# Kernel optimization log

Measured on AMD Instinct MI355X. Metric: run time of the kernel, lower is better.

Reference implementation:

```python
import jax
import jax.numpy as jnp
import numpy as np
from jax import lax

DIM = 512
B, T = 8, 2048
DT = 1.0
DT_REF = 1.0
MAX_GROWTH = 0.3


def _xavier(key, shape):
    fan_in, fan_out = shape[1], shape[0]
    lim = float(np.sqrt(6.0 / (fan_in + fan_out)))
    return jax.random.uniform(key, shape, jnp.float32, -lim, lim)


def setup_inputs() -> dict:
    key = jax.random.key(0)
    ks = jax.random.split(key, 10)
    D = DIM
    return {
        "x": jax.random.normal(ks[0], (B, T, D), jnp.float32),
        # ComplexSVDTransform params (U basis is unused by the transform matrix)
        "v_raw_re": jax.random.normal(ks[1], (D, D), jnp.float32) * 0.02,
        "v_raw_im": jax.random.normal(ks[2], (D, D), jnp.float32) * 0.02,
        "log_sigma": jnp.zeros((D,), jnp.float32),
        "dft_weight": jnp.zeros((), jnp.float32),
        # GlobalFluxTracker params (gate_net only used in forward_step; not here)
        "decay_re": jax.random.normal(ks[3], (D,), jnp.float32) * 0.1 - 1.0,
        "decay_im": jax.random.normal(ks[4], (D,), jnp.float32) * 0.1,
        "mix_w": _xavier(ks[5], (2 * D, 2 * D)),
        "mix_b": jnp.zeros((2 * D,), jnp.float32),
        "proj_w": _xavier(ks[6], (2 * D, 2 * D)),
        "proj_b": jnp.zeros((2 * D,), jnp.float32),
        # TemporalPropagator eigenvalue params
        "lam_re": jax.random.normal(ks[7], (D,), jnp.float32) * 0.01,
        "lam_im": jax.random.normal(ks[8], (D,), jnp.float32) * 0.1,
    }


def _cayley(raw_re, raw_im):
    # Q = (I + A_skew)^{-1} (I - A_skew), A_skew = A - A^H
    A = raw_re + 1j * raw_im
    A_skew = A - A.conj().T
    I = jnp.eye(A.shape[0], dtype=A.dtype)
    return jnp.linalg.solve(I + A_skew, I - A_skew)


def _transform_matrix(v_raw_re, v_raw_im, log_sigma, dft_weight):
    V = _cayley(v_raw_re, v_raw_im)
    S = jnp.exp(log_sigma)
    d = v_raw_re.shape[0]
    n = jnp.arange(d, dtype=jnp.float32)
    k = n[:, None]
    dft = jnp.exp(-2j * jnp.pi * (n * k) / d) / jnp.sqrt(jnp.asarray(d, jnp.float32))
    alpha = jax.nn.sigmoid(dft_weight).astype(jnp.complex64)
    V_scaled = V * S[None, :].astype(V.dtype)  # V @ diag(S)
    return V_scaled * (1.0 - alpha) + dft.astype(jnp.complex64) * alpha


def _scan_combine(c1, c2):
    # s_t = a_t * s_{t-1} + b_t  -> associative combine (later element is c2)
    a1, b1 = c1
    a2, b2 = c2
    return (a1 * a2, b1 * a2 + b2)


def reference(x, v_raw_re, v_raw_im, log_sigma, dft_weight,
              decay_re, decay_im, mix_w, mix_b, proj_w, proj_b,
              lam_re, lam_im):
    D = x.shape[-1]
    # --- encode ---
    W = _transform_matrix(v_raw_re, v_raw_im, log_sigma, dft_weight)  # [D,D] complex
    h = jnp.einsum('btd,de->bte', x.astype(jnp.complex64), W)  # [B,T,D] complex
    # --- flux tracker operators ---
    decay = jax.nn.sigmoid(decay_re) + 1j * decay_im  # [D]
    x_cat = jnp.concatenate([h.real, h.imag], axis=-1)  # [B,T,2D]
    x_in = x_cat @ mix_w.T + mix_b
    x_re, x_im = x_in[..., :D], x_in[..., D:]
    X = x_re + 1j * x_im  # forcing [B,T,D]
    A = jnp.broadcast_to(decay.astype(jnp.complex64), h.shape)  # [B,T,D]
    # --- complex diagonal SSM recurrence via parallel scan ---
    _, states = lax.associative_scan(_scan_combine, (A, X.astype(jnp.complex64)), axis=1)
    # --- project states to source ---
    s_cat = jnp.concatenate([states.real, states.imag], axis=-1)
    s_out = s_cat @ proj_w.T + proj_b
    source = s_out[..., :D] + 1j * s_out[..., D:]
    # --- closed-form transition operators ---
    lam = jnp.clip(lam_re, -MAX_GROWTH, MAX_GROWTH) + 1j * lam_im  # [D]
    exp_arg = lam * (DT / DT_REF)
    t_decay = jnp.exp(exp_arg)
    lam_safe = lam + 1e-8 * jnp.sign(lam.real + 1e-12)
    forcing = (jnp.exp(exp_arg) - 1.0) / lam_safe
    h_out = h * t_decay + source * forcing  # [B,T,D]
    # --- decode ---
    W_inv = jnp.linalg.inv(W)
    x_out = jnp.einsum('btd,de->bte', h_out, W_inv)
    return x_out.real


if __name__ == "__main__":
    out = reference(**setup_inputs())
    print(out.shape, out.dtype)
```

## Files before the change

### kernel.cpp

```cpp
#include <hip/hip_runtime.h>
#include <hip/hip_bf16.h>

typedef unsigned short u16;
typedef _Float16 f16x8 __attribute__((ext_vector_type(8)));
typedef float f32x4 __attribute__((ext_vector_type(4)));

#define DEV __device__ __forceinline__

DEV u16 f2h(float f) { _Float16 h = (_Float16)f; u16 u; __builtin_memcpy(&u, &h, 2); return u; }
DEV float h2f(u16 u) { _Float16 h; __builtin_memcpy(&h, &u, 2); return (float)h; }
DEV void splitf(float v, u16& hi, u16& lo) { hi = f2h(v); lo = f2h(v - h2f(hi)); }
DEV float sigm(float x) { return 1.f / (1.f + __expf(-x)); }
DEV void gload16(const u16* g, u16* l) {
  __builtin_amdgcn_global_load_lds((const __attribute__((address_space(1))) void*)g,
                                   (__attribute__((address_space(3))) void*)l, 16, 0, 0);
}

static const int TT = 2048;

static const size_t OFF_AUG    = 0;
static const size_t OFF_WMAT   = OFF_AUG    + (size_t)512*1024*16;
static const size_t OFF_BINV   = OFF_WMAT   + (size_t)512*512*16;
static const size_t OFF_PIV    = OFF_BINV   + (size_t)64*64*16;
static const size_t OFF_TAB    = OFF_PIV    + (size_t)64*1024*16;
static const size_t OFF_WCATH  = OFF_TAB    + (size_t)512*32;
static const size_t OFF_WCATL  = OFF_WCATH  + (size_t)512*1024*2;
static const size_t OFF_MIXH   = OFF_WCATL  + (size_t)512*1024*2;
static const size_t OFF_MIXL   = OFF_MIXH   + (size_t)1024*1024*2;
static const size_t OFF_PROJH  = OFF_MIXL   + (size_t)1024*1024*2;
static const size_t OFF_PROJL  = OFF_PROJH  + (size_t)1024*1024*2;
static const size_t OFF_B1TH   = OFF_PROJL  + (size_t)1024*1024*2;
static const size_t OFF_B1TL   = OFF_B1TH   + (size_t)512*1024*2;
static const size_t OFF_B2TH   = OFF_B1TL   + (size_t)512*1024*2;
static const size_t OFF_B2TL   = OFF_B2TH   + (size_t)512*1024*2;
static const size_t OFF_BTMIXH = OFF_B2TL   + (size_t)512*1024*2;
static const size_t OFF_BTMIXL = OFF_BTMIXH + (size_t)1024*512*2;
static const size_t OFF_BTFH   = OFF_BTMIXL + (size_t)1024*512*2;
static const size_t OFF_BTFL   = OFF_BTFH   + (size_t)512*1536*2;
static const size_t OFF_BIAS2  = OFF_BTFL   + (size_t)512*1536*2;
static const size_t OFF_CARRY  = OFF_BIAS2  + (size_t)512*4;
static const size_t OFF_PREF   = OFF_CARRY  + (size_t)4096*16*8;
static const size_t OFF_XINF   = OFF_PREF   + (size_t)4096*16*8;
static const size_t OFF_ACATH  = OFF_XINF   + (size_t)16384*1024*4;
static const size_t OFF_ACATL  = OFF_ACATH  + (size_t)16384*1536*2;

__global__ __launch_bounds__(256) void k_split_f32(const float* __restrict__ s, u16* __restrict__ dh,
                                                   u16* __restrict__ dl, int n4) {
  int g = blockIdx.x * 256 + threadIdx.x;
  if (g >= n4) return;
  float4 v = ((const float4*)s)[g];
  ushort4 h, l;
  splitf(v.x, h.x, l.x); splitf(v.y, h.y, l.y); splitf(v.z, h.z, l.z); splitf(v.w, h.w, l.w);
  ((ushort4*)dh)[g] = h;
  ((ushort4*)dl)[g] = l;
}

__global__ __launch_bounds__(256) void k_x_to_acat(const float* __restrict__ x, u16* __restrict__ ah,
                                                   u16* __restrict__ al) {
  int g = blockIdx.x * 256 + threadIdx.x;
  if (g >= 2097152) return;
  float4 v = ((const float4*)x)[g];
  int idx = g * 4;
  int row = idx >> 9, col = idx & 511;
  ushort4 h, l;
  splitf(v.x, h.x, l.x); splitf(v.y, h.y, l.y); splitf(v.z, h.z, l.z); splitf(v.w, h.w, l.w);
  *(ushort4*)(ah + (size_t)row*1536 + col) = h;
  *(ushort4*)(al + (size_t)row*1536 + col) = l;
}

__global__ __launch_bounds__(256) void k_transpose_1024(const float* __restrict__ in, u16* __restrict__ oh,
                                                        u16* __restrict__ ol) {
  __shared__ float s[64][65];
  int lx = threadIdx.x & 63, ly = threadIdx.x >> 6;
#pragma unroll
  for (int i = 0; i < 16; ++i) {
    int c = blockIdx.y*64 + ly*16 + i;
    s[ly*16 + i][lx] = in[(size_t)c*1024 + blockIdx.x*64 + lx];
  }
  __syncthreads();
#pragma unroll
  for (int i = 0; i < 16; ++i) {
    int j = blockIdx.x*64 + ly*16 + i;
    u16 h, l; splitf(s[lx][ly*16 + i], h, l);
    oh[(size_t)j*1024 + blockIdx.y*64 + lx] = h;
    ol[(size_t)j*1024 + blockIdx.y*64 + lx] = l;
  }
}

__global__ __launch_bounds__(256) void k_build_aug_f(const float* __restrict__ vre, const float* __restrict__ vim,
                                                     float2* __restrict__ aug) {
  int g = blockIdx.x * 256 + threadIdx.x;
  if (g >= 512*1024) return;
  int i = g >> 10, j = g & 1023;
  int jc = j & 511;
  float sre = vre[i*512 + jc] - vre[jc*512 + i];
  float sim = vim[i*512 + jc] + vim[jc*512 + i];
  float idd = (i == jc) ? 1.f : 0.f;
  aug[g] = (j < 512) ? make_float2(idd + sre, sim) : make_float2(idd - sre, -sim);
}

template<typename T2, typename TR>
__global__ __launch_bounds__(1024) void gj_inv64_p(const T2* __restrict__ AUG, T2* __restrict__ BINV, int k0) {
  __shared__ T2 mcol[2][64];
  __shared__ T2 praw[2][68];
  const int tid = threadIdx.x;
  const int r = tid >> 4, q = tid & 15;
  T2 a[4];
  const T2* src = AUG + (size_t)(k0 + r)*1024 + k0 + q*4;
#pragma unroll
  for (int jj = 0; jj < 4; ++jj) a[jj] = src[jj];
  if (q == 0) mcol[0][r] = a[0];
  if (r == 0) {
#pragma unroll
    for (int jj = 0; jj < 4; ++jj) { int j = q*4 + jj; praw[0][j + (j >> 4)] = a[jj]; }
  }
  __syncthreads();
  for (int p = 0; p < 64; ++p) {
    const int bu = p & 1;
    T2 pd = praw[bu][p + (p >> 4)];
    TR inv = TR(1) / (pd.x*pd.x + pd.y*pd.y);
    T2 pinv; pinv.x = pd.x*inv; pinv.y = -pd.y*inv;
    T2 mraw = mcol[bu][r];
    T2 g; g.x = mraw.x*pinv.x - mraw.y*pinv.y; g.y = mraw.x*pinv.y + mraw.y*pinv.x;
    if (r == p) {
#pragma unroll
      for (int jj = 0; jj < 4; ++jj) {
        int j = q*4 + jj;
        T2 v;
        if (j == p) v = pinv;
        else { T2 pr = praw[bu][j + (j >> 4)]; v.x = pr.x*pinv.x - pr.y*pinv.y; v.y = pr.x*pinv.y + pr.y*pinv.x; }
        a[jj] = v;
      }
    } else {
#pragma unroll
      for (int jj = 0; jj < 4; ++jj) {
        int j = q*4 + jj;
        if (j == p) { a[jj].x = -g.x; a[jj].y = -g.y; }
        else {
          T2 pr = praw[bu][j + (j >> 4)];
          a[jj].x -= g.x*pr.x - g.y*pr.y;
          a[jj].y -= g.x*pr.y + g.y*pr.x;
        }
      }
    }
    if (p < 63) {
      const int nbu = bu ^ 1;
      if (q == ((p + 1) >> 2)) {
        const int loc = (p + 1) & 3;
#pragma unroll
        for (int jj = 0; jj < 4; ++jj) if (jj == loc) mcol[nbu][r] = a[jj];
      }
      if (r == p + 1) {
#pragma unroll
        for (int jj = 0; jj < 4; ++jj) { int j = q*4 + jj; praw[nbu][j + (j >> 4)] = a[jj]; }
      }
    }
    __syncthreads();
  }
  T2* dst = BINV + (size_t)r*64 + q*4;
#pragma unroll
  for (int jj = 0; jj < 4; ++jj) dst[jj] = a[jj];
}

template<typename T2>
__global__ __launch_bounds__(256) void gj_trans_t(const T2* __restrict__ AUG, const T2* __restrict__ BINV,
                                                  T2* __restrict__ PIV, int k0) {
  __shared__ T2 binv[64][16];
  int tid = threadIdx.x;
  int col  = k0 + 64 + blockIdx.x*64 + (tid & 63);
  int rsub = tid >> 6;
  T2 acc[16];
#pragma unroll
  for (int i = 0; i < 16; ++i) { acc[i].x = 0; acc[i].y = 0; }
  for (int kc = 0; kc < 4; ++kc) {
    for (int l = tid; l < 1024; l += 256) {
      int rr = l >> 4, cc = l & 15;
      binv[rr][cc] = BINV[(size_t)rr*64 + kc*16 + cc];
    }
    __syncthreads();
#pragma unroll 4
    for (int kk = 0; kk < 16; ++kk) {
      T2 av = AUG[(size_t)(k0 + kc*16 + kk)*1024 + col];
#pragma unroll
      for (int i = 0; i < 16; ++i) {
        T2 bv = binv[rsub*16 + i][kk];
        acc[i].x += bv.x*av.x - bv.y*av.y;
        acc[i].y += bv.x*av.y + bv.y*av.x;
      }
    }
    __syncthreads();
  }
#pragma unroll
  for (int i = 0; i < 16; ++i) PIV[(size_t)(rsub*16 + i)*1024 + col] = acc[i];
}

template<typename T2>
__global__ __launch_bounds__(256) void gj_update_t(T2* __restrict__ AUG, const T2* __restrict__ PIV, int k0) {
  __shared__ T2 mult[16][64];
  __shared__ T2 pivc[16][64];
  int tid = threadIdx.x;
  int rb = blockIdx.y;
  int colBase = k0 + 64 + blockIdx.x*64;
  for (int l = tid; l < 1024; l += 256) {
    int rr = l >> 6, kk = l & 63;
    mult[rr][kk] = AUG[(size_t)(rb*16 + rr)*1024 + k0 + kk];
  }
  int ccl = tid & 63, rsub = tid >> 6;
  int col = colBase + ccl;
  T2 acc[4];
#pragma unroll
  for (int i = 0; i < 4; ++i) acc[i] = AUG[(size_t)(rb*16 + rsub*4 + i)*1024 + col];
  for (int kc = 0; kc < 4; ++kc) {
    for (int l = tid; l < 1024; l += 256) {
      int rr = l >> 6, cc = l & 63;
      pivc[rr][cc] = PIV[(size_t)(kc*16 + rr)*1024 + colBase + cc];
    }
    __syncthreads();
#pragma unroll 4
    for (int k2 = 0; k2 < 16; ++k2) {
      int kk = kc*16 + k2;
      T2 pv = pivc[k2][ccl];
#pragma unroll
      for (int i = 0; i < 4; ++i) {
        T2 m = mult[rsub*4 + i][kk];
        acc[i].x -= m.x*pv.x - m.y*pv.y;
        acc[i].y -= m.x*pv.y + m.y*pv.x;
      }
    }
    __syncthreads();
  }
#pragma unroll
  for (int i = 0; i < 4; ++i) {
    int gr = rb*16 + rsub*4 + i;
    T2 o = acc[i];
    if (gr >= k0 && gr < k0 + 64) o = PIV[(size_t)(gr - k0)*1024 + col];
    AUG[(size_t)gr*1024 + col] = o;
  }
}

__global__ __launch_bounds__(256) void k_build_w(const float2* __restrict__ aug, const float* __restrict__ lsig,
                                                 const float* __restrict__ dw, double2* __restrict__ wmat,
                                                 u16* __restrict__ wch, u16* __restrict__ wcl) {
  int g = blockIdx.x * 256 + threadIdx.x;
  if (g >= 512*512) return;
  int k = g >> 9, j = g & 511;
  float2 V = aug[(size_t)k*1024 + 512 + j];
  double S = exp((double)lsig[j]);
  double al = 1.0 / (1.0 + exp(-(double)dw[0]));
  double sc = S * (1.0 - al);
  const float n2pi = (float)(-2.0 * 3.14159265358979323846);
  float nk = (float)(k * j);
  float ph32 = (n2pi * nk) / 512.0f;
  double sn, cs; sincos((double)ph32, &sn, &cs);
  float snf = (float)sn, csf = (float)cs;
  float rsq = sqrtf(512.0f);
  float dre = csf / rsq;
  float dimv = snf / rsq;
  double2 w = make_double2((double)V.x*sc + (double)dre*al, (double)V.y*sc + (double)dimv*al);
  wmat[(size_t)k*512 + j] = w;
  u16 h, l;
  splitf((float)w.x, h, l);
  wch[(size_t)k*1024 + j] = h;  wcl[(size_t)k*1024 + j] = l;
  splitf((float)w.y, h, l);
  wch[(size_t)k*1024 + 512 + j] = h;  wcl[(size_t)k*1024 + 512 + j] = l;
}

__global__ __launch_bounds__(256) void k_build_aug2(const double2* __restrict__ wmat, double2* __restrict__ aug) {
  int g = blockIdx.x * 256 + threadIdx.x;
  if (g >= 512*1024) return;
  int i = g >> 10, j = g & 1023;
  aug[g] = (j < 512) ? wmat[(size_t)i*512 + j] : make_double2((j - 512) == i ? 1.0 : 0.0, 0.0);
}

__global__ __launch_bounds__(256) void k_const512(const float* __restrict__ lamre, const float* __restrict__ lamim,
                                                  double4* __restrict__ tab) {
  int g = blockIdx.x * 256 + threadIdx.x;
  if (g >= 512) return;
  double lr = fmin(fmax((double)lamre[g], -0.3), 0.3);
  double li = (double)lamim[g];
  double e = exp(lr);
  double sn, cs; sincos(li, &sn, &cs);
  double tdre = e*cs, tdim = e*sn;
  double sgn = (lr + 1e-12) >= 0.0 ? 1.0 : -1.0;
  double lsr = lr + 1e-8*sgn, lsi = li;
  double numr = tdre - 1.0, numi = tdim;
  double idn = 1.0 / (lsr*lsr + lsi*lsi);
  double fr = (numr*lsr + numi*lsi)*idn;
  double fi = (numi*lsr - numr*lsi)*idn;
  tab[g] = make_double4(tdre, tdim, fr, fi);
}

__global__ __launch_bounds__(256) void k_build_tb(const double2* __restrict__ aug, const double4* __restrict__ tab,
                                                  u16* __restrict__ b1h, u16* __restrict__ b1l,
                                                  u16* __restrict__ b2h, u16* __restrict__ b2l) {
  int g = blockIdx.x * 256 + threadIdx.x;
  if (g >= 512*512) return;
  int e = g & 511, m = g >> 9;
  double2 wv = aug[(size_t)m*1024 + 512 + e];
  double4 tb = tab[m];
  double twre = tb.x*wv.x - tb.y*wv.y, twim = tb.x*wv.y + tb.y*wv.x;
  double fwre = tb.z*wv.x - tb.w*wv.y, fwim = tb.z*wv.y + tb.w*wv.x;
  u16 h, l;
  splitf((float)twre, h, l);  b1h[(size_t)e*1024 + m] = h;        b1l[(size_t)e*1024 + m] = l;
  splitf((float)-twim, h, l); b1h[(size_t)e*1024 + 512 + m] = h;  b1l[(size_t)e*1024 + 512 + m] = l;
  splitf((float)fwre, h, l);  b2h[(size_t)e*1024 + m] = h;        b2l[(size_t)e*1024 + m] = l;
  splitf((float)-fwim, h, l); b2h[(size_t)e*1024 + 512 + m] = h;  b2l[(size_t)e*1024 + 512 + m] = l;
}

__global__ __launch_bounds__(256) void k_bias2(const double2* __restrict__ aug, const double4* __restrict__ tab,
                                               const float* __restrict__ projb, float* __restrict__ bias2) {
  int e = blockIdx.x;
  int t = threadIdx.x;
  double acc = 0.0;
  for (int d = t; d < 512; d += 256) {
    double2 wv = aug[(size_t)d*1024 + 512 + e];
    double4 tb = tab[d];
    double fwre = tb.z*wv.x - tb.w*wv.y;
    double fwim = tb.z*wv.y + tb.w*wv.x;
    acc += (double)projb[d]*fwre - (double)projb[512 + d]*fwim;
  }
#pragma unroll
  for (int off = 32; off; off >>= 1) acc += __shfl_down(acc, off, 64);
  __shared__ double red[4];
  if ((t & 63) == 0) red[t >> 6] = acc;
  __syncthreads();
  if (t == 0) bias2[e] = (float)(red[0] + red[1] + red[2] + red[3]);
}

template<int K, int NOUT, int EPI, int LDA, int LDO>
__global__ __launch_bounds__(256) void gemm3(const u16* __restrict__ Ah, const u16* __restrict__ Al,
                                             const u16* __restrict__ Bh, const u16* __restrict__ Bl,
                                             u16* __restrict__ outH, u16* __restrict__ outL,
                                             float* __restrict__ outF, const float* __restrict__ bias) {
  __shared__ alignas(16) u16 Ash[128*64];
  __shared__ alignas(16) u16 Asl[128*64];
  __shared__ alignas(16) u16 Bsh[128*64];
  __shared__ alignas(16) u16 Bsl[128*64];
  const int tid = threadIdx.x;
  const int lane = tid & 63, wid = tid >> 6;
  const int wr = wid >> 1, wc = wid & 1;
  const int nwg = gridDim.x * gridDim.y;
  const int flatb = blockIdx.y * gridDim.x + blockIdx.x;
  const int chunk = nwg >> 3;
  const int swz = (flatb & 7) * chunk + (flatb >> 3);
  const int rowTile = (swz / gridDim.x) * 128;
  const int colTile = (swz % gridDim.x) * 128;
  f32x4 zz = {0.f, 0.f, 0.f, 0.f};
  f32x4 acc[4][4];
#pragma unroll
  for (int m = 0; m < 4; ++m)
#pragma unroll
    for (int n = 0; n < 4; ++n) acc[m][n] = zz;

  const int KT = K / 64;
  for (int kt = 0; kt < KT; ++kt) {
    const int k0 = kt * 64;
    __syncthreads();
#pragma unroll
    for (int i = 0; i < 4; ++i) {
      int flat = i*256 + tid;
      int ar = flat >> 3;
      int as = (flat & 7) ^ (ar & 7);
      size_t aoff = (size_t)(rowTile + ar)*LDA + (k0 + as*8);
      size_t boff = (size_t)(colTile + ar)*K   + (k0 + as*8);
      int lb = (i*256 + (tid & ~63)) * 8;
      gload16(Ah + aoff, Ash + lb);
      gload16(Al + aoff, Asl + lb);
      gload16(Bh + boff, Bsh + lb);
      gload16(Bl + boff, Bsl + lb);
    }
    __syncthreads();
#pragma unroll
    for (int ks = 0; ks < 2; ++ks) {
      f16x8 afh[4], afl[4], bfh[4], bfl[4];
#pragma unroll
      for (int m = 0; m < 4; ++m) {
        int row = wr*64 + m*16 + (lane & 15);
        int off = row*128 + (((ks*4 + (lane >> 4)) ^ (row & 7)) << 4);
        afh[m] = *(const f16x8*)((const char*)Ash + off);
        afl[m] = *(const f16x8*)((const char*)Asl + off);
      }
#pragma unroll
      for (int n = 0; n < 4; ++n) {
        int row = wc*64 + n*16 + (lane & 15);
        int off = row*128 + (((ks*4 + (lane >> 4)) ^ (row & 7)) << 4);
        bfh[n] = *(const f16x8*)((const char*)Bsh + off);
        bfl[n] = *(const f16x8*)((const char*)Bsl + off);
      }
#pragma unroll
      for (int m = 0; m < 4; ++m)
#pragma unroll
        for (int n = 0; n < 4; ++n) {
          acc[m][n] = __builtin_amdgcn_mfma_f32_16x16x32_f16(afl[m], bfh[n], acc[m][n], 0, 0, 0);
          acc[m][n] = __builtin_amdgcn_mfma_f32_16x16x32_f16(afh[m], bfl[n], acc[m][n], 0, 0, 0);
          acc[m][n] = __builtin_amdgcn_mfma_f32_16x16x32_f16(afh[m], bfh[n], acc[m][n], 0, 0, 0);
        }
    }
  }
  const int colBase = colTile + wc*64;
  const int rowBase = rowTile + wr*64 + (lane >> 4)*4;
#pragma unroll
  for (int n = 0; n < 4; ++n) {
    int col = colBase + n*16 + (lane & 15);
    float bv = (EPI >= 2) ? bias[col] : 0.f;
#pragma unroll
    for (int m = 0; m < 4; ++m) {
#pragma unroll
      for (int j = 0; j < 4; ++j) {
        int row = rowBase + m*16 + j;
        float v = acc[m][n][j] + bv;
        if (EPI >= 2) {
          outF[(size_t)row*LDO + col] = v;
        } else {
          u16 h, l; splitf(v, h, l);
          outH[(size_t)row*LDO + col] = h;
          outL[(size_t)row*LDO + col] = l;
        }
      }
    }
  }
}

__global__ __launch_bounds__(256) void k_scan1(const float* __restrict__ xin, const float* __restrict__ dre_,
                                               const float* __restrict__ dim_, float2* __restrict__ carry) {
  int g = blockIdx.x * 256 + threadIdx.x;
  int d = g & 511; int rr = g >> 9; int b = rr & 7; int c = rr >> 3;
  float dre = sigm(dre_[d]);
  float dim = dim_[d];
  size_t base = ((size_t)(b*TT + c*128))*1024 + d;
  float sre = 0.f, sim = 0.f;
  for (int t = 0; t < 128; ++t) {
    float xre = xin[base];
    float xim = xin[base + 512];
    float nre = dre*sre - dim*sim + xre;
    float nim = dre*sim + dim*sre + xim;
    sre = nre; sim = nim;
    base += 1024;
  }
  carry[((size_t)(b*512 + d))*16 + c] = make_float2(sre, sim);
}

__global__ __launch_bounds__(256) void k_scan2(const float* __restrict__ dre_, const float* __restrict__ dim_,
                                               const float2* __restrict__ carry, float2* __restrict__ pref) {
  int g = blockIdx.x * 256 + threadIdx.x;
  int d = g & 511; int b = g >> 9;
  float dre = sigm(dre_[d]);
  float dim = dim_[d];
  float are = dre, aim = dim;
#pragma unroll
  for (int i = 0; i < 7; ++i) { float nr = are*are - aim*aim; float ni = 2.f*are*aim; are = nr; aim = ni; }
  float sre = 0.f, sim = 0.f;
  size_t base = ((size_t)(b*512 + d))*16;
  for (int c = 0; c < 16; ++c) {
    pref[base + c] = make_float2(sre, sim);
    float2 cr = carry[base + c];
    float nr = are*sre - aim*sim + cr.x;
    float ni = are*sim + aim*sre + cr.y;
    sre = nr; sim = ni;
  }
}

__global__ __launch_bounds__(256) void k_scan3(const float* __restrict__ xin, const float* __restrict__ dre_,
                                               const float* __restrict__ dim_, const float2* __restrict__ pref,
                                               u16* __restrict__ ah, u16* __restrict__ al) {
  int g = blockIdx.x * 256 + threadIdx.x;
  int d = g & 511; int rr = g >> 9; int b = rr & 7; int c = rr >> 3;
  float dre = sigm(dre_[d]);
  float dim = dim_[d];
  float2 p0 = pref[((size_t)(b*512 + d))*16 + c];
  float sre = p0.x, sim = p0.y;
  size_t base  = ((size_t)(b*TT + c*128))*1024 + d;
  size_t base2 = ((size_t)(b*TT + c*128))*1536 + d;
  for (int t = 0; t < 128; ++t) {
    float xre = xin[base];
    float xim = xin[base + 512];
    float nre = dre*sre - dim*sim + xre;
    float nim = dre*sim + dim*sre + xim;
    sre = nre; sim = nim;
    u16 h, l;
    splitf(sre, h, l); ah[base2 + 512]  = h; al[base2 + 512]  = l;
    splitf(sim, h, l); ah[base2 + 1024] = h; al[base2 + 1024] = l;
    base += 1024; base2 += 1536;
  }
}

extern "C" void kernel_launch(void* const* d_in, const int* in_sizes, int n_in,
                              void* d_out, int out_size, void* d_ws, size_t ws_size,
                              hipStream_t stream) {
  (void)in_sizes; (void)n_in; (void)out_size; (void)ws_size;
  const float* x     = (const float*)d_in[0];
  const float* vre   = (const float*)d_in[1];
  const float* vim   = (const float*)d_in[2];
  const float* lsig  = (const float*)d_in[3];
  const float* dw    = (const float*)d_in[4];
  const float* decre = (const float*)d_in[5];
  const float* decim = (const float*)d_in[6];
  const float* mixw  = (const float*)d_in[7];
  const float* mixb  = (const float*)d_in[8];
  const float* projw = (const float*)d_in[9];
  const float* projb = (const float*)d_in[10];
  const float* lamre = (const float*)d_in[11];
  const float* lamim = (const float*)d_in[12];
  float* out = (float*)d_out;
  char* ws = (char*)d_ws;

  double2* AUG    = (double2*)(ws + OFF_AUG);
  float2*  AUGF   = (float2*)(ws + OFF_AUG);
  double2* WMAT   = (double2*)(ws + OFF_WMAT);
  double2* BINV   = (double2*)(ws + OFF_BINV);
  float2*  BINVF  = (float2*)(ws + OFF_BINV);
  double2* PIV    = (double2*)(ws + OFF_PIV);
  float2*  PIVF   = (float2*)(ws + OFF_PIV);
  double4* TAB    = (double4*)(ws + OFF_TAB);
  u16*    WCATH  = (u16*)(ws + OFF_WCATH);
  u16*    WCATL  = (u16*)(ws + OFF_WCATL);
  u16*    MIXH   = (u16*)(ws + OFF_MIXH);
  u16*    MIXL   = (u16*)(ws + OFF_MIXL);
  u16*    PROJH  = (u16*)(ws + OFF_PROJH);
  u16*    PROJL  = (u16*)(ws + OFF_PROJL);
  u16*    B1TH   = (u16*)(ws + OFF_B1TH);
  u16*    B1TL   = (u16*)(ws + OFF_B1TL);
  u16*    B2TH   = (u16*)(ws + OFF_B2TH);
  u16*    B2TL   = (u16*)(ws + OFF_B2TL);
  u16*    BTMIXH = (u16*)(ws + OFF_BTMIXH);
  u16*    BTMIXL = (u16*)(ws + OFF_BTMIXL);
  u16*    BTFH   = (u16*)(ws + OFF_BTFH);
  u16*    BTFL   = (u16*)(ws + OFF_BTFL);
  float*  BIAS2  = (float*)(ws + OFF_BIAS2);
  float2* CARRY  = (float2*)(ws + OFF_CARRY);
  float2* PREF   = (float2*)(ws + OFF_PREF);
  float*  XINF   = (float*)(ws + OFF_XINF);
  u16*    ACATH  = (u16*)(ws + OFF_ACATH);
  u16*    ACATL  = (u16*)(ws + OFF_ACATL);

  k_const512<<<2, 256, 0, stream>>>(lamre, lamim, TAB);
  k_x_to_acat<<<8192, 256, 0, stream>>>(x, ACATH, ACATL);
  k_split_f32<<<1024, 256, 0, stream>>>(mixw, MIXH, MIXL, 262144);
  k_transpose_1024<<<dim3(16, 16), 256, 0, stream>>>(projw, PROJH, PROJL);

  k_build_aug_f<<<2048, 256, 0, stream>>>(vre, vim, AUGF);
  for (int s = 0; s < 8; ++s) {
    int k0 = s * 64;
    int nb = 15 - s;
    gj_inv64_p<float2, float><<<1, 1024, 0, stream>>>(AUGF, BINVF, k0);
    gj_trans_t<float2><<<nb, 256, 0, stream>>>(AUGF, BINVF, PIVF, k0);
    gj_update_t<float2><<<dim3(nb, 32), 256, 0, stream>>>(AUGF, PIVF, k0);
  }
  k_build_w<<<1024, 256, 0, stream>>>(AUGF, lsig, dw, WMAT, WCATH, WCATL);

  k_build_aug2<<<2048, 256, 0, stream>>>(WMAT, AUG);
  for (int s = 0; s < 8; ++s) {
    int k0 = s * 64;
    int nb = 15 - s;
    gj_inv64_p<double2, double><<<1, 1024, 0, stream>>>(AUG, BINV, k0);
    gj_trans_t<double2><<<nb, 256, 0, stream>>>(AUG, BINV, PIV, k0);
    gj_update_t<double2><<<dim3(nb, 32), 256, 0, stream>>>(AUG, PIV, k0);
  }

  k_build_tb<<<1024, 256, 0, stream>>>(AUG, TAB, B1TH, B1TL, B2TH, B2TL);
  k_bias2<<<512, 256, 0, stream>>>(AUG, TAB, projb, BIAS2);
  gemm3<1024, 512, 0, 1024, 1536><<<dim3(4, 4), 256, 0, stream>>>(B1TH, B1TL, WCATH, WCATL, BTFH, BTFL, nullptr, nullptr);
  gemm3<1024, 1024, 0, 1024, 1536><<<dim3(8, 4), 256, 0, stream>>>(B2TH, B2TL, PROJH, PROJL, BTFH + 512, BTFL + 512, nullptr, nullptr);
  gemm3<1024, 512, 0, 1024, 512><<<dim3(4, 8), 256, 0, stream>>>(MIXH, MIXL, WCATH, WCATL, BTMIXH, BTMIXL, nullptr, nullptr);

  gemm3<512, 1024, 3, 1536, 1024><<<dim3(8, 128), 256, 0, stream>>>(ACATH, ACATL, BTMIXH, BTMIXL, nullptr, nullptr, XINF, mixb);

  k_scan1<<<256, 256, 0, stream>>>(XINF, decre, decim, CARRY);
  k_scan2<<<16, 256, 0, stream>>>(decre, decim, CARRY, PREF);
  k_scan3<<<256, 256, 0, stream>>>(XINF, decre, decim, PREF, ACATH, ACATL);

  gemm3<1536, 512, 2, 1536, 512><<<dim3(4, 128), 256, 0, stream>>>(ACATH, ACATL, BTFH, BTFL, nullptr, nullptr, out, BIAS2);
}
```

Baseline: 2.390 ms.

## Switch Gauss-Jordan inversion to in-place form without augmented identity

Replaces the 512x1024 augmented-matrix Gauss-Jordan inversion with an in-place 512x512 variant. The pivot block column is copied out to a separate buffer each step and receives the block inverse, and work is distributed across all 8 column tiles per step. The Cayley result is now derived as V = 2*(I+A)^{-1} - I, so only one inverse is needed instead of a full solve, and the double-precision augmented build kernel is dropped. This halves the matrix width and the traffic per step. The cost is an extra column-copy pass folded into the pivot kernel, and a different numerical path for V.

```diff
diff --git a/kernel.cpp b/kernel.cpp
--- a/kernel.cpp
+++ b/kernel.cpp
@@ -18,11 +18,12 @@
 
 static const int TT = 2048;
 
-static const size_t OFF_AUG    = 0;
-static const size_t OFF_WMAT   = OFF_AUG    + (size_t)512*1024*16;
-static const size_t OFF_BINV   = OFF_WMAT   + (size_t)512*512*16;
+static const size_t OFF_AUGF   = 0;
+static const size_t OFF_AUG    = OFF_AUGF   + (size_t)512*512*8;
+static const size_t OFF_BINV   = OFF_AUG    + (size_t)512*512*16;
 static const size_t OFF_PIV    = OFF_BINV   + (size_t)64*64*16;
-static const size_t OFF_TAB    = OFF_PIV    + (size_t)64*1024*16;
+static const size_t OFF_MCOPY  = OFF_PIV    + (size_t)64*512*16;
+static const size_t OFF_TAB    = OFF_MCOPY  + (size_t)512*64*16;
 static const size_t OFF_WCATH  = OFF_TAB    + (size_t)512*32;
 static const size_t OFF_WCATL  = OFF_WCATH  + (size_t)512*1024*2;
 static const size_t OFF_MIXH   = OFF_WCATL  + (size_t)512*1024*2;
@@ -90,23 +91,31 @@
 __global__ __launch_bounds__(256) void k_build_aug_f(const float* __restrict__ vre, const float* __restrict__ vim,
                                                      float2* __restrict__ aug) {
   int g = blockIdx.x * 256 + threadIdx.x;
-  if (g >= 512*1024) return;
-  int i = g >> 10, j = g & 1023;
-  int jc = j & 511;
-  float sre = vre[i*512 + jc] - vre[jc*512 + i];
-  float sim = vim[i*512 + jc] + vim[jc*512 + i];
-  float idd = (i == jc) ? 1.f : 0.f;
-  aug[g] = (j < 512) ? make_float2(idd + sre, sim) : make_float2(idd - sre, -sim);
+  if (g >= 512*512) return;
+  int i = g >> 9, j = g & 511;
+  float sre = vre[i*512 + j] - vre[j*512 + i];
+  float sim = vim[i*512 + j] + vim[j*512 + i];
+  float idd = (i == j) ? 1.f : 0.f;
+  aug[g] = make_float2(idd + sre, sim);
 }
 
 template<typename T2, typename TR>
-__global__ __launch_bounds__(1024) void gj_inv64_p(const T2* __restrict__ AUG, T2* __restrict__ BINV, int k0) {
+__global__ __launch_bounds__(1024) void gj_inv64_p(const T2* __restrict__ AUG, T2* __restrict__ BINV,
+                                                   T2* __restrict__ MCOPY, int k0) {
+  if (blockIdx.x > 0) {
+    int b = blockIdx.x - 1;
+    for (int l = threadIdx.x; l < 4096; l += 1024) {
+      int rr = l >> 6, cc = l & 63;
+      MCOPY[(size_t)(b*64 + rr)*64 + cc] = AUG[(size_t)(b*64 + rr)*512 + k0 + cc];
+    }
+    return;
+  }
   __shared__ T2 mcol[2][64];
   __shared__ T2 praw[2][68];
   const int tid = threadIdx.x;
   const int r = tid >> 4, q = tid & 15;
   T2 a[4];
-  const T2* src = AUG + (size_t)(k0 + r)*1024 + k0 + q*4;
+  const T2* src = AUG + (size_t)(k0 + r)*512 + k0 + q*4;
 #pragma unroll
   for (int jj = 0; jj < 4; ++jj) a[jj] = src[jj];
   if (q == 0) mcol[0][r] = a[0];
@@ -164,10 +173,11 @@
 
 template<typename T2>
 __global__ __launch_bounds__(256) void gj_trans_t(const T2* __restrict__ AUG, const T2* __restrict__ BINV,
-                                                  T2* __restrict__ PIV, int k0) {
+                                                  T2* __restrict__ PIV, int k0, int s) {
   __shared__ T2 binv[64][16];
   int tid = threadIdx.x;
-  int col  = k0 + 64 + blockIdx.x*64 + (tid & 63);
+  int cj = blockIdx.x + (blockIdx.x >= s ? 1 : 0);
+  int col = cj*64 + (tid & 63);
   int rsub = tid >> 6;
   T2 acc[16];
 #pragma unroll
@@ -180,7 +190,7 @@
     __syncthreads();
 #pragma unroll 4
     for (int kk = 0; kk < 16; ++kk) {
-      T2 av = AUG[(size_t)(k0 + kc*16 + kk)*1024 + col];
+      T2 av = AUG[(size_t)(k0 + kc*16 + kk)*512 + col];
 #pragma unroll
       for (int i = 0; i < 16; ++i) {
         T2 bv = binv[rsub*16 + i][kk];
@@ -191,38 +201,48 @@
     __syncthreads();
   }
 #pragma unroll
-  for (int i = 0; i < 16; ++i) PIV[(size_t)(rsub*16 + i)*1024 + col] = acc[i];
+  for (int i = 0; i < 16; ++i) PIV[(size_t)(rsub*16 + i)*512 + col] = acc[i];
 }
 
 template<typename T2>
-__global__ __launch_bounds__(256) void gj_update_t(T2* __restrict__ AUG, const T2* __restrict__ PIV, int k0) {
+__global__ __launch_bounds__(256) void gj_update_t(T2* __restrict__ AUG, const T2* __restrict__ PIV,
+                                                   const T2* __restrict__ BINV, const T2* __restrict__ MCOPY,
+                                                   int k0) {
   __shared__ T2 mult[16][64];
   __shared__ T2 pivc[16][64];
   int tid = threadIdx.x;
   int rb = blockIdx.y;
-  int colBase = k0 + 64 + blockIdx.x*64;
+  int cj = blockIdx.x;
+  const int s = k0 >> 6;
+  const bool ispiv = (cj == s);
+  int colBase = cj*64;
   for (int l = tid; l < 1024; l += 256) {
     int rr = l >> 6, kk = l & 63;
-    mult[rr][kk] = AUG[(size_t)(rb*16 + rr)*1024 + k0 + kk];
+    mult[rr][kk] = MCOPY[(size_t)(rb*16 + rr)*64 + kk];
   }
   int ccl = tid & 63, rsub = tid >> 6;
   int col = colBase + ccl;
   T2 acc[4];
-#pragma unroll
-  for (int i = 0; i < 4; ++i) acc[i] = AUG[(size_t)(rb*16 + rsub*4 + i)*1024 + col];
+  if (ispiv) {
+#pragma unroll
+    for (int i = 0; i < 4; ++i) { acc[i].x = 0; acc[i].y = 0; }
+  } else {
+#pragma unroll
+    for (int i = 0; i < 4; ++i) acc[i] = AUG[(size_t)(rb*16 + rsub*4 + i)*512 + col];
+  }
   for (int kc = 0; kc < 4; ++kc) {
     for (int l = tid; l < 1024; l += 256) {
       int rr = l >> 6, cc = l & 63;
-      pivc[rr][cc] = PIV[(size_t)(kc*16 + rr)*1024 + colBase + cc];
+      pivc[rr][cc] = ispiv ? BINV[(size_t)(kc*16 + rr)*64 + cc]
+                           : PIV[(size_t)(kc*16 + rr)*512 + colBase + cc];
     }
     __syncthreads();
 #pragma unroll 4
     for (int k2 = 0; k2 < 16; ++k2) {
-      int kk = kc*16 + k2;
       T2 pv = pivc[k2][ccl];
 #pragma unroll
       for (int i = 0; i < 4; ++i) {
-        T2 m = mult[rsub*4 + i][kk];
+        T2 m = mult[rsub*4 + i][kc*16 + k2];
         acc[i].x -= m.x*pv.x - m.y*pv.y;
         acc[i].y -= m.x*pv.y + m.y*pv.x;
       }
@@ -233,18 +253,22 @@
   for (int i = 0; i < 4; ++i) {
     int gr = rb*16 + rsub*4 + i;
     T2 o = acc[i];
-    if (gr >= k0 && gr < k0 + 64) o = PIV[(size_t)(gr - k0)*1024 + col];
-    AUG[(size_t)gr*1024 + col] = o;
-  }
-}
-
-__global__ __launch_bounds__(256) void k_build_w(const float2* __restrict__ aug, const float* __restrict__ lsig,
-                                                 const float* __restrict__ dw, double2* __restrict__ wmat,
+    if (gr >= k0 && gr < k0 + 64) {
+      o = ispiv ? BINV[(size_t)(gr - k0)*64 + ccl] : PIV[(size_t)(gr - k0)*512 + col];
+    }
+    AUG[(size_t)gr*512 + col] = o;
+  }
+}
+
+__global__ __launch_bounds__(256) void k_build_w(const float2* __restrict__ augf, const float* __restrict__ lsig,
+                                                 const float* __restrict__ dw, double2* __restrict__ w64,
                                                  u16* __restrict__ wch, u16* __restrict__ wcl) {
   int g = blockIdx.x * 256 + threadIdx.x;
   if (g >= 512*512) return;
   int k = g >> 9, j = g & 511;
-  float2 V = aug[(size_t)k*1024 + 512 + j];
+  float2 Z = augf[(size_t)k*512 + j];
+  double Vre = 2.0*(double)Z.x - ((k == j) ? 1.0 : 0.0);
+  double Vim = 2.0*(double)Z.y;
   double S = exp((double)lsig[j]);
   double al = 1.0 / (1.0 + exp(-(double)dw[0]));
   double sc = S * (1.0 - al);
@@ -256,20 +280,13 @@
   float rsq = sqrtf(512.0f);
   float dre = csf / rsq;
   float dimv = snf / rsq;
-  double2 w = make_double2((double)V.x*sc + (double)dre*al, (double)V.y*sc + (double)dimv*al);
-  wmat[(size_t)k*512 + j] = w;
+  double2 w = make_double2(Vre*sc + (double)dre*al, Vim*sc + (double)dimv*al);
+  w64[(size_t)k*512 + j] = w;
   u16 h, l;
   splitf((float)w.x, h, l);
   wch[(size_t)k*1024 + j] = h;  wcl[(size_t)k*1024 + j] = l;
   splitf((float)w.y, h, l);
   wch[(size_t)k*1024 + 512 + j] = h;  wcl[(size_t)k*1024 + 512 + j] = l;
-}
-
-__global__ __launch_bounds__(256) void k_build_aug2(const double2* __restrict__ wmat, double2* __restrict__ aug) {
-  int g = blockIdx.x * 256 + threadIdx.x;
-  if (g >= 512*1024) return;
-  int i = g >> 10, j = g & 1023;
-  aug[g] = (j < 512) ? wmat[(size_t)i*512 + j] : make_double2((j - 512) == i ? 1.0 : 0.0, 0.0);
 }
 
 __global__ __launch_bounds__(256) void k_const512(const float* __restrict__ lamre, const float* __restrict__ lamim,
@@ -290,13 +307,13 @@
   tab[g] = make_double4(tdre, tdim, fr, fi);
 }
 
-__global__ __launch_bounds__(256) void k_build_tb(const double2* __restrict__ aug, const double4* __restrict__ tab,
+__global__ __launch_bounds__(256) void k_build_tb(const double2* __restrict__ winv, const double4* __restrict__ tab,
                                                   u16* __restrict__ b1h, u16* __restrict__ b1l,
                                                   u16* __restrict__ b2h, u16* __restrict__ b2l) {
   int g = blockIdx.x * 256 + threadIdx.x;
   if (g >= 512*512) return;
   int e = g & 511, m = g >> 9;
-  double2 wv = aug[(size_t)m*1024 + 512 + e];
+  double2 wv = winv[(size_t)m*512 + e];
   double4 tb = tab[m];
   double twre = tb.x*wv.x - tb.y*wv.y, twim = tb.x*wv.y + tb.y*wv.x;
   double fwre = tb.z*wv.x - tb.w*wv.y, fwim = tb.z*wv.y + tb.w*wv.x;
@@ -307,13 +324,13 @@
   splitf((float)-fwim, h, l); b2h[(size_t)e*1024 + 512 + m] = h;  b2l[(size_t)e*1024 + 512 + m] = l;
 }
 
-__global__ __launch_bounds__(256) void k_bias2(const double2* __restrict__ aug, const double4* __restrict__ tab,
+__global__ __launch_bounds__(256) void k_bias2(const double2* __restrict__ winv, const double4* __restrict__ tab,
                                                const float* __restrict__ projb, float* __restrict__ bias2) {
   int e = blockIdx.x;
   int t = threadIdx.x;
   double acc = 0.0;
   for (int d = t; d < 512; d += 256) {
-    double2 wv = aug[(size_t)d*1024 + 512 + e];
+    double2 wv = winv[(size_t)d*512 + e];
     double4 tb = tab[d];
     double fwre = tb.z*wv.x - tb.w*wv.y;
     double fwim = tb.z*wv.y + tb.w*wv.x;
@@ -504,13 +521,14 @@
   float* out = (float*)d_out;
   char* ws = (char*)d_ws;
 
+  float2*  AUGF   = (float2*)(ws + OFF_AUGF);
   double2* AUG    = (double2*)(ws + OFF_AUG);
-  float2*  AUGF   = (float2*)(ws + OFF_AUG);
-  double2* WMAT   = (double2*)(ws + OFF_WMAT);
   double2* BINV   = (double2*)(ws + OFF_BINV);
   float2*  BINVF  = (float2*)(ws + OFF_BINV);
   double2* PIV    = (double2*)(ws + OFF_PIV);
   float2*  PIVF   = (float2*)(ws + OFF_PIV);
+  double2* MCOPY  = (double2*)(ws + OFF_MCOPY);
+  float2*  MCOPYF = (float2*)(ws + OFF_MCOPY);
   double4* TAB    = (double4*)(ws + OFF_TAB);
   u16*    WCATH  = (u16*)(ws + OFF_WCATH);
   u16*    WCATL  = (u16*)(ws + OFF_WCATL);
@@ -538,23 +556,20 @@
   k_split_f32<<<1024, 256, 0, stream>>>(mixw, MIXH, MIXL, 262144);
   k_transpose_1024<<<dim3(16, 16), 256, 0, stream>>>(projw, PROJH, PROJL);
 
-  k_build_aug_f<<<2048, 256, 0, stream>>>(vre, vim, AUGF);
+  k_build_aug_f<<<1024, 256, 0, stream>>>(vre, vim, AUGF);
   for (int s = 0; s < 8; ++s) {
     int k0 = s * 64;
-    int nb = 15 - s;
-    gj_inv64_p<float2, float><<<1, 1024, 0, stream>>>(AUGF, BINVF, k0);
-    gj_trans_t<float2><<<nb, 256, 0, stream>>>(AUGF, BINVF, PIVF, k0);
-    gj_update_t<float2><<<dim3(nb, 32), 256, 0, stream>>>(AUGF, PIVF, k0);
-  }
-  k_build_w<<<1024, 256, 0, stream>>>(AUGF, lsig, dw, WMAT, WCATH, WCATL);
-
-  k_build_aug2<<<2048, 256, 0, stream>>>(WMAT, AUG);
+    gj_inv64_p<float2, float><<<9, 1024, 0, stream>>>(AUGF, BINVF, MCOPYF, k0);
+    gj_trans_t<float2><<<7, 256, 0, stream>>>(AUGF, BINVF, PIVF, k0, s);
+    gj_update_t<float2><<<dim3(8, 32), 256, 0, stream>>>(AUGF, PIVF, BINVF, MCOPYF, k0);
+  }
+  k_build_w<<<1024, 256, 0, stream>>>(AUGF, lsig, dw, AUG, WCATH, WCATL);
+
   for (int s = 0; s < 8; ++s) {
     int k0 = s * 64;
-    int nb = 15 - s;
-    gj_inv64_p<double2, double><<<1, 1024, 0, stream>>>(AUG, BINV, k0);
-    gj_trans_t<double2><<<nb, 256, 0, stream>>>(AUG, BINV, PIV, k0);
-    gj_update_t<double2><<<dim3(nb, 32), 256, 0, stream>>>(AUG, PIV, k0);
+    gj_inv64_p<double2, double><<<9, 1024, 0, stream>>>(AUG, BINV, MCOPY, k0);
+    gj_trans_t<double2><<<7, 256, 0, stream>>>(AUG, BINV, PIV, k0, s);
+    gj_update_t<double2><<<dim3(8, 32), 256, 0, stream>>>(AUG, PIV, BINV, MCOPY, k0);
   }
 
   k_build_tb<<<1024, 256, 0, stream>>>(AUG, TAB, B1TH, B1TL, B2TH, B2TL);
```

Result: faster. 2.341 ms, median of 3 (-2.1%).
